# Optimization experiments

Measured on AMD Instinct MI355X. Metric: run time of the kernel, lower is better.

Reference implementation:

```python
import jax, jax.numpy as jnp
import numpy as np

B, T_FRAMES, N, D, H, HT = 2, 16, 256, 768, 12, 12
INNER = 2 * D  # ConditionedTransitionBlock expansion_factor=2

def _ln(x, eps=1e-5):
    m = jnp.mean(x, axis=-1, keepdims=True)
    v = jnp.var(x, axis=-1, keepdims=True)
    return (x - m) * jax.lax.rsqrt(v + eps)

def _adaln(a, s, snorm_w, scale_w, scale_b, shift_w):
    an = _ln(a)            # LayerNorm(dim), no affine
    sn = _ln(s) * snorm_w  # LayerNorm(dim_cond), weight only
    return jax.nn.sigmoid(sn @ scale_w + scale_b) * an + sn @ shift_w

def _forward(a, s, bias, timestamps,
             ada_snorm_w, ada_scale_w, ada_scale_b, ada_shift_w,
             pb_q_w, pb_q_b, pb_k_w, pb_v_w, pb_g_w, pb_o_w,
             op_w, op_b,
             tr_snorm_w, tr_scale_w, tr_scale_b, tr_shift_w,
             tr_gate_w, tr_ab_w, tr_ba_w, tr_out_w, tr_out_b,
             tmp_ln_w, tmp_ln_b, tmp_q_w, tmp_q_b, tmp_k_w, tmp_v_w,
             tmp_decay, tmp_o_w,
             mask, multiplicity, T):
    BT, Nn, Dd = a.shape
    Bb = BT // T
    dh = Dd // H
    # --- AdaLN ---
    b = _adaln(a, s, ada_snorm_w, ada_scale_w, ada_scale_b, ada_shift_w)
    # --- pair-bias spatial attention (compute_pair_bias=False: z already (B,N,N,H)) ---
    q = (b @ pb_q_w + pb_q_b).reshape(BT, Nn, H, dh)
    k = (b @ pb_k_w).reshape(BT, Nn, H, dh)
    v = (b @ pb_v_w).reshape(BT, Nn, H, dh)
    z = jnp.transpose(bias, (0, 3, 1, 2))     # (B, H, N, N)
    z = jnp.repeat(z, multiplicity, axis=0)   # expand over T -> (B*T, H, N, N)
    scores = jnp.einsum('bqhd,bkhd->bhqk', q, k) * (dh ** -0.5) + z
    scores = jnp.where(mask[:, None, None, :], scores, -1e6)
    attn = jax.nn.softmax(scores, axis=-1)
    o = jnp.einsum('bhqk,bkhd->bqhd', attn, v).reshape(BT, Nn, Dd)
    g = jax.nn.sigmoid(b @ pb_g_w)
    attn_out = (g * o) @ pb_o_w
    # gated output projection (sigmoid, weights init 0 / bias -2) multiplied into residual
    a = a + jax.nn.sigmoid(s @ op_w + op_b) * attn_out
    # --- temporal attention with decay over T frames ---
    x = a.reshape(Bb, T, Nn, Dd).transpose(0, 2, 1, 3)   # (B, N, T, D)
    h = _ln(x) * tmp_ln_w + tmp_ln_b
    dht = Dd // HT
    qt = (h @ tmp_q_w + tmp_q_b).reshape(Bb, Nn, T, HT, dht)
    kt = (h @ tmp_k_w).reshape(Bb, Nn, T, HT, dht)
    vt = (h @ tmp_v_w).reshape(Bb, Nn, T, HT, dht)
    dt = jnp.abs(timestamps[:, :, None] - timestamps[:, None, :])           # (B, T, T)
    tb = -jax.nn.softplus(tmp_decay)[None, :, None, None] * dt[:, None]     # (B, HT, T, T)
    sct = jnp.einsum('bnqhd,bnkhd->bnhqk', qt, kt) * (dht ** -0.5) + tb[:, None]
    att = jax.nn.softmax(sct, axis=-1)
    ot = jnp.einsum('bnhqk,bnkhd->bnqhd', att, vt).reshape(Bb, Nn, T, Dd) @ tmp_o_w
    x = x + ot  # residual inside temporal attention
    a = x.transpose(0, 2, 1, 3).reshape(BT, Nn, Dd)
    # --- conditioned transition (SwiGLU gated by sigmoid(Linear(s))) ---
    b2 = _adaln(a, s, tr_snorm_w, tr_scale_w, tr_scale_b, tr_shift_w)
    hid = jax.nn.silu(b2 @ tr_gate_w) * (b2 @ tr_ab_w)
    a = a + jax.nn.sigmoid(s @ tr_out_w + tr_out_b) * (hid @ tr_ba_w)
    return a  # post_layer_norm=False -> Identity

def setup_inputs():
    key = jax.random.key(0)
    ks = iter(jax.random.split(key, 48))
    f = lambda shape, sc=1.0: jax.random.normal(next(ks), shape, jnp.float32) * sc
    return {
        'a': f((B * T_FRAMES, N, D)),
        's': f((B * T_FRAMES, N, D)),
        'bias': f((B, N, N, H)),
        'mask': jnp.ones((B * T_FRAMES, N), dtype=bool),
        'timestamps': jnp.sort(jax.random.uniform(next(ks), (B, T_FRAMES)) * 10.0, axis=-1),
        'multiplicity': T_FRAMES,
        'T': T_FRAMES,
        'ada_snorm_w': jnp.ones((D,)), 'ada_scale_w': f((D, D), 0.02),
        'ada_scale_b': jnp.zeros((D,)), 'ada_shift_w': f((D, D), 0.02),
        'pb_q_w': f((D, D), 0.02), 'pb_q_b': jnp.zeros((D,)),
        'pb_k_w': f((D, D), 0.02), 'pb_v_w': f((D, D), 0.02),
        'pb_g_w': f((D, D), 0.02), 'pb_o_w': f((D, D), 0.02),
        'op_w': f((D, D), 0.02), 'op_b': jnp.full((D,), -2.0),
        'tr_snorm_w': jnp.ones((D,)), 'tr_scale_w': f((D, D), 0.02),
        'tr_scale_b': jnp.zeros((D,)), 'tr_shift_w': f((D, D), 0.02),
        'tr_gate_w': f((D, INNER), 0.02), 'tr_ab_w': f((D, INNER), 0.02),
        'tr_ba_w': f((INNER, D), 0.02),
        'tr_out_w': f((D, D), 0.02), 'tr_out_b': jnp.full((D,), -2.0),
        'tmp_ln_w': jnp.ones((D,)), 'tmp_ln_b': jnp.zeros((D,)),
        'tmp_q_w': f((D, D), 0.02), 'tmp_q_b': jnp.zeros((D,)),
        'tmp_k_w': f((D, D), 0.02), 'tmp_v_w': f((D, D), 0.02),
        'tmp_decay': jnp.full((HT,), 0.5), 'tmp_o_w': f((D, D), 0.02),
    }

def reference(a, s, bias, mask, timestamps, multiplicity, T,
              ada_snorm_w, ada_scale_w, ada_scale_b, ada_shift_w,
              pb_q_w, pb_q_b, pb_k_w, pb_v_w, pb_g_w, pb_o_w,
              op_w, op_b,
              tr_snorm_w, tr_scale_w, tr_scale_b, tr_shift_w,
              tr_gate_w, tr_ab_w, tr_ba_w, tr_out_w, tr_out_b,
              tmp_ln_w, tmp_ln_b, tmp_q_w, tmp_q_b, tmp_k_w, tmp_v_w,
              tmp_decay, tmp_o_w):
    return _forward(a, s, bias, timestamps,
                    ada_snorm_w, ada_scale_w, ada_scale_b, ada_shift_w,
                    pb_q_w, pb_q_b, pb_k_w, pb_v_w, pb_g_w, pb_o_w,
                    op_w, op_b,
                    tr_snorm_w, tr_scale_w, tr_scale_b, tr_shift_w,
                    tr_gate_w, tr_ab_w, tr_ba_w, tr_out_w, tr_out_b,
                    tmp_ln_w, tmp_ln_b, tmp_q_w, tmp_q_b, tmp_k_w, tmp_v_w,
                    tmp_decay, tmp_o_w,
                    mask, multiplicity, T)
```

## Files before the change

kernel.cpp:

```cpp
#include <hip/hip_runtime.h>

typedef short s16x8 __attribute__((ext_vector_type(8)));
typedef short s16x4 __attribute__((ext_vector_type(4)));
typedef float f32x4 __attribute__((ext_vector_type(4)));
typedef __bf16 bf16x8 __attribute__((ext_vector_type(8)));

__device__ __forceinline__ float bf2f(short u) {
  union { unsigned int i; float f; } c;
  c.i = ((unsigned int)(unsigned short)u) << 16;
  return c.f;
}
__device__ __forceinline__ short f2bf(float f) {
  union { float f; unsigned int i; } c; c.f = f;
  unsigned int r = c.i + 0x7FFFu + ((c.i >> 16) & 1u);
  return (short)(r >> 16);
}
__device__ __forceinline__ float sigmoidf_(float x) { return 1.f / (1.f + __expf(-x)); }

template <typename T>
__device__ __forceinline__ auto mfma_sel(T a, T b, f32x4 c, int)
    -> decltype(__builtin_amdgcn_mfma_f32_16x16x32_bf16(a, b, c, 0, 0, 0)) {
  return __builtin_amdgcn_mfma_f32_16x16x32_bf16(a, b, c, 0, 0, 0);
}
template <typename T>
__device__ __forceinline__ f32x4 mfma_sel(T a, T b, f32x4 c, long) {
  return __builtin_amdgcn_mfma_f32_16x16x32_bf16(
      __builtin_bit_cast(bf16x8, a), __builtin_bit_cast(bf16x8, b), c, 0, 0, 0);
}
__device__ __forceinline__ f32x4 MFMA16(s16x8 a, s16x8 b, f32x4 c) {
  return mfma_sel(a, b, c, 0);
}

__device__ __forceinline__ void gl2lds16(const void* g, void* l) {
  __builtin_amdgcn_global_load_lds(
      (const __attribute__((address_space(1))) unsigned int*)g,
      (__attribute__((address_space(3))) unsigned int*)l, 16, 0, 0);
}

#define OFF_WADA1    0u
#define OFF_WQKVG    2359296u
#define OFF_WO       7077888u
#define OFF_WGATES   8257536u
#define OFF_WTMPQKV  10616832u
#define OFF_WTMPO    14155776u
#define OFF_WADA2    15335424u
#define OFF_WTRANS   17694720u
#define OFF_WBA      22413312u
#define OFF_BIAS     24772608u
#define OFF_ZT       24812544u
#define OFF_AN1      31104000u
#define OFF_SN1      43686912u
#define OFF_SN2      56269824u
#define OFF_SBF      68852736u
#define OFF_CADA     81435648u
#define OFF_QKVG     106601472u
#define OFF_GATES    156933120u
#define OFF_OGO      182098944u
#define OFF_A1       194681856u

__global__ __launch_bounds__(256) void prep_all(
    const float* p0, const float* p1, const float* p2, const float* p3,
    const float* p4, const float* p5, const float* p6, const float* p7,
    const float* p8, const float* p9, const float* p10, const float* p11,
    const float* p12, const float* p13, const float* p14, const float* p15,
    const float* p16, const float* p17, short* wsb,
    const float* __restrict__ zsrc, const float* __restrict__ ada_scale_b,
    const float* __restrict__ pb_q_b, const float* __restrict__ op_b,
    const float* __restrict__ tr_out_b, const float* __restrict__ tmp_q_b,
    const float* __restrict__ tr_scale_b,
    float* __restrict__ biasbuf, short* __restrict__ zt,
    const float* __restrict__ a_in, const float* __restrict__ s_in,
    const float* __restrict__ lnw1, const float* __restrict__ lnw2,
    short* __restrict__ an1, short* __restrict__ sn1, short* __restrict__ sn2,
    short* __restrict__ sbf) {
  const int z = blockIdx.z;
  const int tid = threadIdx.y * 32 + threadIdx.x;
  if (z < 18) {
    struct E { int K, N, dst; };
    const E tab[18] = {
        {768, 768, 0},        {768, 768, 589824},
        {768, 768, 1179648},  {768, 768, 1769472},
        {768, 768, 2359296},  {768, 768, 2949120},
        {768, 768, 3538944},
        {768, 768, 4128768},  {768, 768, 4718592},
        {768, 768, 7667712},  {768, 768, 8257536},
        {768, 1536, 8847360}, {768, 1536, 10027008},
        {1536, 768, 11206656},
        {768, 768, 5308416},  {768, 768, 5898240}, {768, 768, 6488064},
        {768, 768, 7077888}};
    int K = tab[z].K, N = tab[z].N;
    int n0 = blockIdx.x << 5, k0 = blockIdx.y << 5;
    if (n0 >= N || k0 >= K) return;
    const float* src;
    switch (z) {
      case 0: src = p0; break;  case 1: src = p1; break;
      case 2: src = p2; break;  case 3: src = p3; break;
      case 4: src = p4; break;  case 5: src = p5; break;
      case 6: src = p6; break;  case 7: src = p7; break;
      case 8: src = p8; break;  case 9: src = p9; break;
      case 10: src = p10; break; case 11: src = p11; break;
      case 12: src = p12; break; case 13: src = p13; break;
      case 14: src = p14; break; case 15: src = p15; break;
      case 16: src = p16; break; default: src = p17; break;
    }
    short* dst = wsb + tab[z].dst;
    __shared__ float tile[32][33];
    int tx = threadIdx.x, ty = threadIdx.y;
#pragma unroll
    for (int j = 0; j < 4; j++)
      tile[ty + j * 8][tx] = src[(long)(k0 + ty + j * 8) * N + n0 + tx];
    __syncthreads();
#pragma unroll
    for (int j = 0; j < 4; j++)
      dst[(long)(n0 + ty + j * 8) * K + k0 + tx] = f2bf(tile[tx][ty + j * 8]);
  } else if (z == 18) {
    const int bid = blockIdx.y * 48 + blockIdx.x;
    if (bid < 512) {
      const int b = bid >> 8, qq = bid & 255;
      const float* src = zsrc + (long)bid * 3072 + tid * 12;
      f32x4 v0 = *(const f32x4*)(src);
      f32x4 v1 = *(const f32x4*)(src + 4);
      f32x4 v2 = *(const f32x4*)(src + 8);
      float vals[12] = {v0[0], v0[1], v0[2], v0[3], v1[0], v1[1],
                        v1[2], v1[3], v2[0], v2[1], v2[2], v2[3]};
#pragma unroll
      for (int h = 0; h < 12; h++)
        zt[(((long)(b * 12 + h) * 256 + qq) << 8) + tid] = f2bf(vals[h]);
    } else if (bid < 551) {
      int j = (bid - 512) * 256 + tid;
      if (j < 9984) {
        float v;
        if (j < 1536) v = (j < 768) ? ada_scale_b[j] : 0.f;
        else if (j < 4608) { int jj = j - 1536; v = (jj < 768) ? pb_q_b[jj] : 0.f; }
        else if (j < 6144) { int jj = j - 4608; v = (jj < 768) ? op_b[jj] : tr_out_b[jj - 768]; }
        else if (j < 8448) { int jj = j - 6144; v = (jj < 768) ? tmp_q_b[jj] : 0.f; }
        else { int jj = j - 8448; v = (jj < 768) ? tr_scale_b[jj] : 0.f; }
        biasbuf[j] = v;
      }
    }
  } else {
    const int bid = blockIdx.y * 48 + blockIdx.x;
    if (bid >= 2048) return;
    const int wave = tid >> 6, lane = tid & 63;
    const int row = (bid << 2) + wave;
    const float* ar = a_in + (long)row * 768;
    const float* sr = s_in + (long)row * 768;
    f32x4 av[3], sv[3];
    float s0 = 0, s1 = 0, s2 = 0, s3 = 0;
#pragma unroll
    for (int k = 0; k < 3; k++) {
      int col = (lane << 2) + (k << 8);
      av[k] = *(const f32x4*)(ar + col);
      sv[k] = *(const f32x4*)(sr + col);
#pragma unroll
      for (int e = 0; e < 4; e++) {
        s0 += av[k][e]; s1 += av[k][e] * av[k][e];
        s2 += sv[k][e]; s3 += sv[k][e] * sv[k][e];
      }
    }
#pragma unroll
    for (int o = 32; o; o >>= 1) {
      s0 += __shfl_xor(s0, o, 64); s1 += __shfl_xor(s1, o, 64);
      s2 += __shfl_xor(s2, o, 64); s3 += __shfl_xor(s3, o, 64);
    }
    const float inv768 = 1.f / 768.f;
    float ma = s0 * inv768, va = s1 * inv768 - ma * ma;
    float ia = rsqrtf(va + 1e-5f);
    float ms = s2 * inv768, vs = s3 * inv768 - ms * ms;
    float is_ = rsqrtf(vs + 1e-5f);
#pragma unroll
    for (int k = 0; k < 3; k++) {
      int col = (lane << 2) + (k << 8);
      long o = (long)row * 768 + col;
      s16x4 o1, o2, o3, o4;
#pragma unroll
      for (int e = 0; e < 4; e++) {
        o1[e] = f2bf((av[k][e] - ma) * ia);
        float sn = (sv[k][e] - ms) * is_;
        o2[e] = f2bf(sn * lnw1[col + e]);
        o3[e] = f2bf(sn * lnw2[col + e]);
        o4[e] = f2bf(sv[k][e]);
      }
      *(s16x4*)(an1 + o) = o1;
      *(s16x4*)(sn1 + o) = o2;
      *(s16x4*)(sn2 + o) = o3;
      *(s16x4*)(sbf + o) = o4;
    }
  }
}

__global__ __launch_bounds__(256) void ln_affine(
    const float* __restrict__ in, const float* __restrict__ w,
    const float* __restrict__ b, short* __restrict__ out) {
  const int wave = threadIdx.x >> 6, lane = threadIdx.x & 63;
  const int row = (blockIdx.x << 2) + wave;
  const float* xr = in + (long)row * 768;
  f32x4 xv[3];
  float s0 = 0, s1 = 0;
#pragma unroll
  for (int k = 0; k < 3; k++) {
    int col = (lane << 2) + (k << 8);
    xv[k] = *(const f32x4*)(xr + col);
#pragma unroll
    for (int e = 0; e < 4; e++) { s0 += xv[k][e]; s1 += xv[k][e] * xv[k][e]; }
  }
#pragma unroll
  for (int o = 32; o; o >>= 1) { s0 += __shfl_xor(s0, o, 64); s1 += __shfl_xor(s1, o, 64); }
  const float inv768 = 1.f / 768.f;
  float m = s0 * inv768, v = s1 * inv768 - m * m;
  float inv = rsqrtf(v + 1e-5f);
#pragma unroll
  for (int k = 0; k < 3; k++) {
    int col = (lane << 2) + (k << 8);
    s16x4 p;
#pragma unroll
    for (int e = 0; e < 4; e++) {
      float y = (xv[k][e] - m) * inv;
      if (w) y = y * w[col + e] + b[col + e];
      p[e] = f2bf(y);
    }
    *(s16x4*)(out + (long)row * 768 + col) = p;
  }
}

template <int EP>
__device__ __forceinline__ void dev_gemm_bt(
    short* lds,
    const short* __restrict__ A, const short* __restrict__ W,
    const float* __restrict__ bias, void* __restrict__ Cout,
    const float* __restrict__ res, const short* __restrict__ gate,
    int K, int ldA, int ldC, int gld) {
  short* sA = lds;
  short* sB = lds + 8192;
  const int tid = threadIdx.x;
  const int wave = tid >> 6, lane = tid & 63;
  const int m0 = blockIdx.y << 7;
  const int n0 = blockIdx.x << 7;
  const int wm = (wave & 1) << 6, wn = (wave >> 1) << 6;
  const int q = lane >> 4, r = lane & 15;
  f32x4 acc[4][4];
#pragma unroll
  for (int i = 0; i < 4; i++)
#pragma unroll
    for (int j = 0; j < 4; j++) acc[i][j] = (f32x4){0.f, 0.f, 0.f, 0.f};

  for (int kt = 0; kt < K; kt += 64) {
    __syncthreads();
#pragma unroll
    for (int t = 0; t < 4; t++) {
      int c = (t << 8) + tid;
      int m = c >> 3, kc = (c & 7) ^ (m & 7);
      gl2lds16(A + (long)(m0 + m) * ldA + kt + (kc << 3),
               sA + (((t << 8) + (wave << 6)) << 3));
      gl2lds16(W + (long)(n0 + m) * K + kt + (kc << 3),
               sB + (((t << 8) + (wave << 6)) << 3));
    }
    __syncthreads();
#pragma unroll
    for (int ks = 0; ks < 2; ks++) {
      s16x8 av[4], bv[4];
#pragma unroll
      for (int mt = 0; mt < 4; mt++) {
        int row = wm + (mt << 4) + r;
        int ch = ((ks << 2) + q) ^ (row & 7);
        av[mt] = *(const s16x8*)(sA + ((row << 3) + ch) * 8);
      }
#pragma unroll
      for (int nt = 0; nt < 4; nt++) {
        int row = wn + (nt << 4) + r;
        int ch = ((ks << 2) + q) ^ (row & 7);
        bv[nt] = *(const s16x8*)(sB + ((row << 3) + ch) * 8);
      }
#pragma unroll
      for (int mt = 0; mt < 4; mt++)
#pragma unroll
        for (int nt = 0; nt < 4; nt++)
          acc[mt][nt] = MFMA16(bv[nt], av[mt], acc[mt][nt]);
    }
  }
#pragma unroll
  for (int mt = 0; mt < 4; mt++) {
    const int gm = m0 + wm + (mt << 4) + r;
#pragma unroll
    for (int nt = 0; nt < 4; nt++) {
      const int gnb = n0 + wn + (nt << 4) + (q << 2);
      f32x4 v = acc[mt][nt];
      if (bias) {
        f32x4 b4 = *(const f32x4*)(bias + gnb);
        v += b4;
      }
      long o = (long)gm * ldC + gnb;
      if (EP == 0) {
        s16x4 p;
#pragma unroll
        for (int e = 0; e < 4; e++) p[e] = f2bf(v[e]);
        *(s16x4*)((short*)Cout + o) = p;
      } else if (EP == 1) {
        s16x4 p;
#pragma unroll
        for (int e = 0; e < 4; e++) p[e] = f2bf(sigmoidf_(v[e]));
        *(s16x4*)((short*)Cout + o) = p;
      } else if (EP == 2) {
        f32x4 r4 = *(const f32x4*)(res + o);
        *(f32x4*)((float*)Cout + o) = r4 + v;
      } else {
        f32x4 r4 = *(const f32x4*)(res + o);
        s16x4 g4 = *(const s16x4*)(gate + (long)gm * gld + gnb);
        f32x4 out;
#pragma unroll
        for (int e = 0; e < 4; e++) out[e] = r4[e] + bf2f(g4[e]) * v[e];
        *(f32x4*)((float*)Cout + o) = out;
      }
    }
  }
}

template <int MODE>
__device__ __forceinline__ void dev_gemm_dual(
    short* lds,
    const short* __restrict__ A, const short* __restrict__ W, int woff2,
    const float* __restrict__ bias, const short* __restrict__ an,
    short* __restrict__ out, int ldO) {
  short* sA = lds;
  short* sB1 = lds + 8192;
  short* sB2 = lds + 12288;
  const int tid = threadIdx.x;
  const int wave = tid >> 6, lane = tid & 63;
  const int m0 = blockIdx.y << 7;
  const int n0 = blockIdx.x << 6;
  const int wm = (wave & 1) << 6, wn = (wave >> 1) << 5;
  const int q = lane >> 4, r = lane & 15;
  f32x4 acc1[4][2], acc2[4][2];
#pragma unroll
  for (int i = 0; i < 4; i++)
#pragma unroll
    for (int j = 0; j < 2; j++) {
      acc1[i][j] = (f32x4){0.f, 0.f, 0.f, 0.f};
      acc2[i][j] = (f32x4){0.f, 0.f, 0.f, 0.f};
    }

  for (int kt = 0; kt < 768; kt += 64) {
    __syncthreads();
#pragma unroll
    for (int t = 0; t < 4; t++) {
      int c = (t << 8) + tid;
      int m = c >> 3, kc = (c & 7) ^ (m & 7);
      gl2lds16(A + (long)(m0 + m) * 768 + kt + (kc << 3),
               sA + (((t << 8) + (wave << 6)) << 3));
    }
#pragma unroll
    for (int t = 0; t < 2; t++) {
      int c = (t << 8) + tid;
      int rb = c >> 3, kc = (c & 7) ^ (rb & 7);
      gl2lds16(W + (long)(n0 + rb) * 768 + kt + (kc << 3),
               sB1 + (((t << 8) + (wave << 6)) << 3));
      gl2lds16(W + (long)(woff2 + n0 + rb) * 768 + kt + (kc << 3),
               sB2 + (((t << 8) + (wave << 6)) << 3));
    }
    __syncthreads();
#pragma unroll
    for (int ks = 0; ks < 2; ks++) {
      s16x8 av[4], b1[2], b2[2];
#pragma unroll
      for (int mt = 0; mt < 4; mt++) {
        int row = wm + (mt << 4) + r;
        int ch = ((ks << 2) + q) ^ (row & 7);
        av[mt] = *(const s16x8*)(sA + ((row << 3) + ch) * 8);
      }
#pragma unroll
      for (int nt = 0; nt < 2; nt++) {
        int row = wn + (nt << 4) + r;
        int ch = ((ks << 2) + q) ^ (row & 7);
        b1[nt] = *(const s16x8*)(sB1 + ((row << 3) + ch) * 8);
        b2[nt] = *(const s16x8*)(sB2 + ((row << 3) + ch) * 8);
      }
#pragma unroll
      for (int mt = 0; mt < 4; mt++)
#pragma unroll
        for (int nt = 0; nt < 2; nt++) {
          acc1[mt][nt] = MFMA16(b1[nt], av[mt], acc1[mt][nt]);
          acc2[mt][nt] = MFMA16(b2[nt], av[mt], acc2[mt][nt]);
        }
    }
  }
#pragma unroll
  for (int mt = 0; mt < 4; mt++) {
    const int gm = m0 + wm + (mt << 4) + r;
#pragma unroll
    for (int nt = 0; nt < 2; nt++) {
      const int gnb = n0 + wn + (nt << 4) + (q << 2);
      s16x4 p;
      if (MODE == 0) {
        f32x4 b4 = *(const f32x4*)(bias + gnb);
        s16x4 an4 = *(const s16x4*)(an + (long)gm * 768 + gnb);
#pragma unroll
        for (int e = 0; e < 4; e++)
          p[e] = f2bf(sigmoidf_(acc1[mt][nt][e] + b4[e]) * bf2f(an4[e]) +
                      acc2[mt][nt][e]);
      } else {
#pragma unroll
        for (int e = 0; e < 4; e++) {
          float x = acc1[mt][nt][e];
          p[e] = f2bf(x * sigmoidf_(x) * acc2[mt][nt][e]);
        }
      }
      *(s16x4*)(out + (long)gm * ldO + gnb) = p;
    }
  }
}

template <int EP>
__global__ __launch_bounds__(256) void gemm_bt(
    const short* __restrict__ A, const short* __restrict__ W,
    const float* __restrict__ bias, void* __restrict__ Cout,
    const float* __restrict__ res, const short* __restrict__ gate,
    int K, int ldA, int ldC, int gld) {
  __shared__ short lds[16384];
  dev_gemm_bt<EP>(lds, A, W, bias, Cout, res, gate, K, ldA, ldC, gld);
}

template <int MODE>
__global__ __launch_bounds__(256) void gemm_dual(
    const short* __restrict__ A, const short* __restrict__ W, int woff2,
    const float* __restrict__ bias, const short* __restrict__ an,
    short* __restrict__ out, int ldO) {
  __shared__ short lds[16384];
  dev_gemm_dual<MODE>(lds, A, W, woff2, bias, an, out, ldO);
}

__global__ __launch_bounds__(256) void gemm_pair(
    const short* __restrict__ sbf, const short* __restrict__ wgates,
    const float* __restrict__ bias_g, short* __restrict__ gates,
    const short* __restrict__ sn1, const short* __restrict__ wada1,
    const float* __restrict__ bias_a, const short* __restrict__ an1,
    short* __restrict__ outb) {
  __shared__ short lds[16384];
  if (blockIdx.z == 0)
    dev_gemm_bt<1>(lds, sbf, wgates, bias_g, (void*)gates, nullptr, nullptr,
                   768, 768, 1536, 0);
  else
    dev_gemm_dual<0>(lds, sn1, wada1, 768, bias_a, an1, outb, 768);
}

__global__ __launch_bounds__(256) void attn_spatial(
    const short* __restrict__ qkvg, const short* __restrict__ zt, short* __restrict__ ogo) {
  __shared__ short sKP[256 * 64];
  __shared__ short sVt[64 * 256];
  const int tid = threadIdx.x;
  const int wave = tid >> 6, lane = tid & 63;
  const int qt = blockIdx.x, h = blockIdx.y, bt = blockIdx.z;
  const int b = bt >> 4;
  const int q0 = qt << 6;
  const long rowbase = (long)bt << 8;
  const int hoff = h << 6;

#pragma unroll
  for (int t = 0; t < 8; t++) {
    int c = (t << 8) + tid;
    int tok = c >> 3, kc = (c & 7) ^ (tok & 7);
    *(s16x8*)(sKP + (c << 3)) =
        *(const s16x8*)(qkvg + (rowbase + tok) * 3072 + 768 + hoff + (kc << 3));
  }
#pragma unroll
  for (int t = 0; t < 8; t++) {
    int u = (t << 8) + tid;
    int tok = u >> 3, dc = u & 7;
    s16x8 v8 = *(const s16x8*)(qkvg + (rowbase + tok) * 3072 + 1536 + hoff + (dc << 3));
#pragma unroll
    for (int e = 0; e < 8; e++) {
      int d = (dc << 3) + e;
      int ch = (tok >> 3) ^ (d & 7);
      sVt[((d << 5) + ch) * 8 + (tok & 7)] = v8[e];
    }
  }
  __syncthreads();

  const int q = lane >> 4, cc = lane & 15;
  f32x4 acc[16];
#pragma unroll
  for (int i = 0; i < 16; i++) acc[i] = (f32x4){0.f, 0.f, 0.f, 0.f};
  {
    const int arow = (wave << 4) + cc;
    const short* qrow = qkvg + (rowbase + q0 + arow) * 3072 + hoff;
#pragma unroll
    for (int ks = 0; ks < 2; ks++) {
      s16x8 av = *(const s16x8*)(qrow + (ks << 5) + (q << 3));
#pragma unroll
      for (int nt = 0; nt < 16; nt++) {
        int tok = (nt << 4) + cc;
        int chb = ((ks << 2) + q) ^ (tok & 7);
        s16x8 bv = *(const s16x8*)(sKP + ((tok << 3) + chb) * 8);
        acc[nt] = MFMA16(av, bv, acc[nt]);
      }
    }
  }
  const short* ztb = zt + (((long)(b * 12 + h) * 256 + q0 + (wave << 4)) << 8);
#pragma unroll
  for (int reg = 0; reg < 4; reg++) {
    int lr = (q << 2) + reg;
    float mx = -3.0e38f;
#pragma unroll
    for (int nt = 0; nt < 16; nt++) {
      float v = acc[nt][reg] * 0.125f + bf2f(ztb[lr * 256 + (nt << 4) + cc]);
      acc[nt][reg] = v;
      mx = fmaxf(mx, v);
    }
    mx = fmaxf(mx, __shfl_xor(mx, 1, 16));
    mx = fmaxf(mx, __shfl_xor(mx, 2, 16));
    mx = fmaxf(mx, __shfl_xor(mx, 4, 16));
    mx = fmaxf(mx, __shfl_xor(mx, 8, 16));
    float sum = 0.f;
#pragma unroll
    for (int nt = 0; nt < 16; nt++) {
      float e = __expf(acc[nt][reg] - mx);
      acc[nt][reg] = e; sum += e;
    }
    sum += __shfl_xor(sum, 1, 16);
    sum += __shfl_xor(sum, 2, 16);
    sum += __shfl_xor(sum, 4, 16);
    sum += __shfl_xor(sum, 8, 16);
    float inv = 1.f / sum;
#pragma unroll
    for (int nt = 0; nt < 16; nt++) acc[nt][reg] *= inv;
  }
  __syncthreads();
#pragma unroll
  for (int nt = 0; nt < 16; nt++) {
#pragma unroll
    for (int reg = 0; reg < 4; reg++) {
      int rP = (wave << 4) + (q << 2) + reg;
      int col = (nt << 4) + cc;
      int ch = (col >> 3) ^ (rP & 7);
      sKP[((rP << 5) + ch) * 8 + (col & 7)] = f2bf(acc[nt][reg]);
    }
  }
  __syncthreads();
  f32x4 oacc[4];
#pragma unroll
  for (int i = 0; i < 4; i++) oacc[i] = (f32x4){0.f, 0.f, 0.f, 0.f};
  const int prow = (wave << 4) + cc;
#pragma unroll
  for (int ksi = 0; ksi < 8; ksi++) {
    int cha = ((ksi << 2) + q) ^ (prow & 7);
    s16x8 pa = *(const s16x8*)(sKP + ((prow << 5) + cha) * 8);
#pragma unroll
    for (int dt = 0; dt < 4; dt++) {
      int d = (dt << 4) + cc;
      int chv = ((ksi << 2) + q) ^ (d & 7);
      s16x8 bv = *(const s16x8*)(sVt + ((d << 5) + chv) * 8);
      oacc[dt] = MFMA16(pa, bv, oacc[dt]);
    }
  }
#pragma unroll
  for (int dt = 0; dt < 4; dt++) {
#pragma unroll
    for (int reg = 0; reg < 4; reg++) {
      int rowt = q0 + (wave << 4) + (q << 2) + reg;
      int dcol = (dt << 4) + cc;
      long grow = rowbase + rowt;
      float gl = bf2f(qkvg[grow * 3072 + 2304 + hoff + dcol]);
      ogo[grow * 768 + hoff + dcol] = f2bf(oacc[dt][reg] * sigmoidf_(gl));
    }
  }
}

__global__ __launch_bounds__(256) void attn_temporal(
    const short* __restrict__ qkvt, const float* __restrict__ ts,
    const float* __restrict__ decay_raw, short* __restrict__ out) {
  __shared__ short sKV[16 * 1544];
  const int bn = blockIdx.x;
  const int b = bn >> 8, n = bn & 255;
  const int tid = threadIdx.x;
#pragma unroll
  for (int t = 0; t < 12; t++) {
    int u = t * 256 + tid;
    int row = u / 192, cc = u % 192;
    *(s16x8*)(sKV + row * 1544 + cc * 8) =
        *(const s16x8*)(qkvt + ((long)(b * 16 + row) * 256 + n) * 2304 + 768 + cc * 8);
  }
  __syncthreads();
  const int h = tid >> 4, tq = tid & 15;
  if (h < 12) {
    const int hoff = h << 6;
    float dec = log1pf(__expf(decay_raw[h]));
    float tsq = ts[b * 16 + tq];
    s16x8 qv[8];
    const short* qrow = qkvt + ((long)(b * 16 + tq) * 256 + n) * 2304 + hoff;
#pragma unroll
    for (int dc = 0; dc < 8; dc++) qv[dc] = *(const s16x8*)(qrow + dc * 8);
    float sc[16];
#pragma unroll
    for (int tk = 0; tk < 16; tk++) {
      float dot = 0.f;
#pragma unroll
      for (int dc = 0; dc < 8; dc++) {
        s16x8 kv = *(const s16x8*)(sKV + tk * 1544 + hoff + dc * 8);
#pragma unroll
        for (int e = 0; e < 8; e++) dot += bf2f(qv[dc][e]) * bf2f(kv[e]);
      }
      sc[tk] = dot * 0.125f - dec * fabsf(tsq - ts[b * 16 + tk]);
    }
    float mx = sc[0];
#pragma unroll
    for (int tk = 1; tk < 16; tk++) mx = fmaxf(mx, sc[tk]);
    float sum = 0.f;
#pragma unroll
    for (int tk = 0; tk < 16; tk++) { sc[tk] = __expf(sc[tk] - mx); sum += sc[tk]; }
    float inv = 1.f / sum;
    float oa[64];
#pragma unroll
    for (int d = 0; d < 64; d++) oa[d] = 0.f;
#pragma unroll
    for (int tk = 0; tk < 16; tk++) {
      float wgt = sc[tk] * inv;
#pragma unroll
      for (int dc = 0; dc < 8; dc++) {
        s16x8 vv = *(const s16x8*)(sKV + tk * 1544 + 768 + hoff + dc * 8);
#pragma unroll
        for (int e = 0; e < 8; e++) oa[dc * 8 + e] += wgt * bf2f(vv[e]);
      }
    }
    long orow = (long)(b * 16 + tq) * 256 + n;
#pragma unroll
    for (int dc = 0; dc < 8; dc++) {
      s16x8 o8;
#pragma unroll
      for (int e = 0; e < 8; e++) o8[e] = f2bf(oa[dc * 8 + e]);
      *(s16x8*)(out + orow * 768 + hoff + dc * 8) = o8;
    }
  }
}

extern "C" void kernel_launch(void* const* d_in, const int* in_sizes, int n_in,
                              void* d_out, int out_size, void* d_ws, size_t ws_size,
                              hipStream_t stream) {
  (void)in_sizes; (void)n_in; (void)out_size; (void)ws_size;
  const float* a_in      = (const float*)d_in[0];
  const float* s_in      = (const float*)d_in[1];
  const float* bias_in   = (const float*)d_in[2];
  const float* ts        = (const float*)d_in[4];
  const float* ada_snorm = (const float*)d_in[7];
  const float* ada_scale_w = (const float*)d_in[8];
  const float* ada_scale_b = (const float*)d_in[9];
  const float* ada_shift_w = (const float*)d_in[10];
  const float* pb_q_w = (const float*)d_in[11];
  const float* pb_q_b = (const float*)d_in[12];
  const float* pb_k_w = (const float*)d_in[13];
  const float* pb_v_w = (const float*)d_in[14];
  const float* pb_g_w = (const float*)d_in[15];
  const float* pb_o_w = (const float*)d_in[16];
  const float* op_w = (const float*)d_in[17];
  const float* op_b = (const float*)d_in[18];
  const float* tr_snorm = (const float*)d_in[19];
  const float* tr_scale_w = (const float*)d_in[20];
  const float* tr_scale_b = (const float*)d_in[21];
  const float* tr_shift_w = (const float*)d_in[22];
  const float* tr_gate_w = (const float*)d_in[23];
  const float* tr_ab_w = (const float*)d_in[24];
  const float* tr_ba_w = (const float*)d_in[25];
  const float* tr_out_w = (const float*)d_in[26];
  const float* tr_out_b = (const float*)d_in[27];
  const float* tmp_ln_w = (const float*)d_in[28];
  const float* tmp_ln_b = (const float*)d_in[29];
  const float* tmp_q_w = (const float*)d_in[30];
  const float* tmp_q_b = (const float*)d_in[31];
  const float* tmp_k_w = (const float*)d_in[32];
  const float* tmp_v_w = (const float*)d_in[33];
  const float* tmp_decay = (const float*)d_in[34];
  const float* tmp_o_w = (const float*)d_in[35];

  char* ws = (char*)d_ws;
  short* W16 = (short*)ws;
  short* WADA1 = (short*)(ws + OFF_WADA1);
  short* WQKVG = (short*)(ws + OFF_WQKVG);
  short* WO = (short*)(ws + OFF_WO);
  short* WGATES = (short*)(ws + OFF_WGATES);
  short* WTMPQKV = (short*)(ws + OFF_WTMPQKV);
  short* WTMPO = (short*)(ws + OFF_WTMPO);
  short* WADA2 = (short*)(ws + OFF_WADA2);
  short* WTRANS = (short*)(ws + OFF_WTRANS);
  short* WBA = (short*)(ws + OFF_WBA);
  float* BIASB = (float*)(ws + OFF_BIAS);
  short* ZT = (short*)(ws + OFF_ZT);
  short* AN1 = (short*)(ws + OFF_AN1);
  short* SN1 = (short*)(ws + OFF_SN1);
  short* SN2 = (short*)(ws + OFF_SN2);
  short* SBF = (short*)(ws + OFF_SBF);
  short* CADA = (short*)(ws + OFF_CADA);
  short* QKVG = (short*)(ws + OFF_QKVG);
  short* GATES = (short*)(ws + OFF_GATES);
  short* OGO = (short*)(ws + OFF_OGO);
  float* A1F = (float*)(ws + OFF_A1);
  float* OUTF = (float*)d_out;

  prep_all<<<dim3(48, 48, 20), dim3(32, 8, 1), 0, stream>>>(
      ada_scale_w, ada_shift_w, pb_q_w, pb_k_w, pb_v_w, pb_g_w, pb_o_w,
      op_w, tr_out_w, tr_scale_w, tr_shift_w, tr_gate_w, tr_ab_w, tr_ba_w,
      tmp_q_w, tmp_k_w, tmp_v_w, tmp_o_w, W16,
      bias_in, ada_scale_b, pb_q_b, op_b, tr_out_b, tmp_q_b, tr_scale_b,
      BIASB, ZT,
      a_in, s_in, ada_snorm, tr_snorm, AN1, SN1, SN2, SBF);
  gemm_pair<<<dim3(12, 64, 2), 256, 0, stream>>>(
      SBF, WGATES, BIASB + 4608, GATES, SN1, WADA1, BIASB + 0, AN1, SBF);
  gemm_bt<0><<<dim3(24, 64), 256, 0, stream>>>(SBF, WQKVG, BIASB + 1536, QKVG,
                                               nullptr, nullptr, 768, 768, 3072, 0);
  attn_spatial<<<dim3(4, 12, 32), 256, 0, stream>>>(QKVG, ZT, OGO);
  gemm_bt<3><<<dim3(6, 64), 256, 0, stream>>>(OGO, WO, nullptr, A1F, a_in, GATES,
                                              768, 768, 768, 1536);
  ln_affine<<<2048, 256, 0, stream>>>(A1F, tmp_ln_w, tmp_ln_b, AN1);
  gemm_bt<0><<<dim3(18, 64), 256, 0, stream>>>(AN1, WTMPQKV, BIASB + 6144, QKVG,
                                               nullptr, nullptr, 768, 768, 2304, 0);
  attn_temporal<<<512, 256, 0, stream>>>(QKVG, ts, tmp_decay, OGO);
  gemm_bt<2><<<dim3(6, 64), 256, 0, stream>>>(OGO, WTMPO, nullptr, A1F, A1F, nullptr,
                                              768, 768, 768, 0);
  ln_affine<<<2048, 256, 0, stream>>>(A1F, nullptr, nullptr, SN1);
  gemm_dual<0><<<dim3(12, 64), 256, 0, stream>>>(SN2, WADA2, 768, BIASB + 8448, SN1,
                                                 SBF, 768);
  gemm_dual<1><<<dim3(24, 64), 256, 0, stream>>>(SBF, WTRANS, 1536, nullptr, nullptr,
                                                 CADA, 1536);
  gemm_bt<3><<<dim3(6, 64), 256, 0, stream>>>(CADA, WBA, nullptr, OUTF, A1F,
                                              GATES + 768, 1536, 1536, 768, 1536);
}
```

Measured before the change: 680.3 us.

## Store GEMM operands in MFMA-fragment packed layout and drop LDS staging

Activation and weight matrices are written by the producers in a packed 16-row x 8-column tile layout that matches the MFMA fragment order. The GEMM kernels then load each fragment straight from global memory with one 16-byte vector load per lane, with no LDS staging and no __syncthreads. This removes the LDS round trip and the barriers. In exchange, the A and B tiles are no longer shared through LDS, so every wave fetches its own fragments from global/L2 with no software prefetch, which may raise global traffic and expose load latency.

```diff
diff --git a/kernel.cpp b/kernel.cpp
--- a/kernel.cpp
+++ b/kernel.cpp
@@ -31,10 +31,8 @@
   return mfma_sel(a, b, c, 0);
 }
 
-__device__ __forceinline__ void gl2lds16(const void* g, void* l) {
-  __builtin_amdgcn_global_load_lds(
-      (const __attribute__((address_space(1))) unsigned int*)g,
-      (__attribute__((address_space(3))) unsigned int*)l, 16, 0, 0);
+__device__ __forceinline__ long upk(int m, int c, int nu) {
+  return ((long)(m >> 4) * nu + (c >> 3)) * 128 + ((m & 15) << 3) + (c & 7);
 }
 
 #define OFF_WADA1    0u
@@ -104,6 +102,7 @@
       case 16: src = p16; break; default: src = p17; break;
     }
     short* dst = wsb + tab[z].dst;
+    const int ku = K >> 3;
     __shared__ float tile[32][33];
     int tx = threadIdx.x, ty = threadIdx.y;
 #pragma unroll
@@ -111,8 +110,10 @@
       tile[ty + j * 8][tx] = src[(long)(k0 + ty + j * 8) * N + n0 + tx];
     __syncthreads();
 #pragma unroll
-    for (int j = 0; j < 4; j++)
-      dst[(long)(n0 + ty + j * 8) * K + k0 + tx] = f2bf(tile[tx][ty + j * 8]);
+    for (int j = 0; j < 4; j++) {
+      int n = n0 + ty + j * 8, k = k0 + tx;
+      dst[upk(n, k, ku)] = f2bf(tile[tx][ty + j * 8]);
+    }
   } else if (z == 18) {
     const int bid = blockIdx.y * 48 + blockIdx.x;
     if (bid < 512) {
@@ -171,7 +172,7 @@
 #pragma unroll
     for (int k = 0; k < 3; k++) {
       int col = (lane << 2) + (k << 8);
-      long o = (long)row * 768 + col;
+      long o = upk(row, col, 96);
       s16x4 o1, o2, o3, o4;
 #pragma unroll
       for (int e = 0; e < 4; e++) {
@@ -219,25 +220,30 @@
       if (w) y = y * w[col + e] + b[col + e];
       p[e] = f2bf(y);
     }
-    *(s16x4*)(out + (long)row * 768 + col) = p;
+    *(s16x4*)(out + upk(row, col, 96)) = p;
   }
 }
 
 template <int EP>
-__device__ __forceinline__ void dev_gemm_bt(
-    short* lds,
+__device__ __forceinline__ void dev_gemm_pk(
     const short* __restrict__ A, const short* __restrict__ W,
     const float* __restrict__ bias, void* __restrict__ Cout,
     const float* __restrict__ res, const short* __restrict__ gate,
-    int K, int ldA, int ldC, int gld) {
-  short* sA = lds;
-  short* sB = lds + 8192;
+    int K, int ldC, int gld) {
   const int tid = threadIdx.x;
   const int wave = tid >> 6, lane = tid & 63;
-  const int m0 = blockIdx.y << 7;
-  const int n0 = blockIdx.x << 7;
+  const int m0 = blockIdx.y << 7, n0 = blockIdx.x << 7;
   const int wm = (wave & 1) << 6, wn = (wave >> 1) << 6;
   const int q = lane >> 4, r = lane & 15;
+  const int ku = K >> 3;
+  const short* ap[4];
+  const short* bp[4];
+#pragma unroll
+  for (int mt = 0; mt < 4; mt++)
+    ap[mt] = A + (long)(((m0 + wm) >> 4) + mt) * ku * 128 + (lane << 3);
+#pragma unroll
+  for (int nt = 0; nt < 4; nt++)
+    bp[nt] = W + (long)(((n0 + wn) >> 4) + nt) * ku * 128 + (lane << 3);
   f32x4 acc[4][4];
 #pragma unroll
   for (int i = 0; i < 4; i++)
@@ -245,38 +251,25 @@
     for (int j = 0; j < 4; j++) acc[i][j] = (f32x4){0.f, 0.f, 0.f, 0.f};
 
   for (int kt = 0; kt < K; kt += 64) {
-    __syncthreads();
-#pragma unroll
-    for (int t = 0; t < 4; t++) {
-      int c = (t << 8) + tid;
-      int m = c >> 3, kc = (c & 7) ^ (m & 7);
-      gl2lds16(A + (long)(m0 + m) * ldA + kt + (kc << 3),
-               sA + (((t << 8) + (wave << 6)) << 3));
-      gl2lds16(W + (long)(n0 + m) * K + kt + (kc << 3),
-               sB + (((t << 8) + (wave << 6)) << 3));
-    }
-    __syncthreads();
 #pragma unroll
     for (int ks = 0; ks < 2; ks++) {
       s16x8 av[4], bv[4];
 #pragma unroll
-      for (int mt = 0; mt < 4; mt++) {
-        int row = wm + (mt << 4) + r;
-        int ch = ((ks << 2) + q) ^ (row & 7);
-        av[mt] = *(const s16x8*)(sA + ((row << 3) + ch) * 8);
-      }
-#pragma unroll
-      for (int nt = 0; nt < 4; nt++) {
-        int row = wn + (nt << 4) + r;
-        int ch = ((ks << 2) + q) ^ (row & 7);
-        bv[nt] = *(const s16x8*)(sB + ((row << 3) + ch) * 8);
-      }
+      for (int mt = 0; mt < 4; mt++)
+        av[mt] = *(const s16x8*)(ap[mt] + (ks << 9));
+#pragma unroll
+      for (int nt = 0; nt < 4; nt++)
+        bv[nt] = *(const s16x8*)(bp[nt] + (ks << 9));
 #pragma unroll
       for (int mt = 0; mt < 4; mt++)
 #pragma unroll
         for (int nt = 0; nt < 4; nt++)
           acc[mt][nt] = MFMA16(bv[nt], av[mt], acc[mt][nt]);
     }
+#pragma unroll
+    for (int mt = 0; mt < 4; mt++) ap[mt] += 1024;
+#pragma unroll
+    for (int nt = 0; nt < 4; nt++) bp[nt] += 1024;
   }
 #pragma unroll
   for (int mt = 0; mt < 4; mt++) {
@@ -316,20 +309,27 @@
 }
 
 template <int MODE>
-__device__ __forceinline__ void dev_gemm_dual(
-    short* lds,
-    const short* __restrict__ A, const short* __restrict__ W, int woff2,
-    const float* __restrict__ bias, const short* __restrict__ an,
-    short* __restrict__ out, int ldO) {
-  short* sA = lds;
-  short* sB1 = lds + 8192;
-  short* sB2 = lds + 12288;
+__device__ __forceinline__ void dev_gemm_dual_pk(
+    const short* __restrict__ A, const short* __restrict__ W1,
+    const short* __restrict__ W2, const float* __restrict__ bias,
+    const short* __restrict__ an, short* __restrict__ out, int nuO) {
   const int tid = threadIdx.x;
   const int wave = tid >> 6, lane = tid & 63;
-  const int m0 = blockIdx.y << 7;
-  const int n0 = blockIdx.x << 6;
+  const int m0 = blockIdx.y << 7, n0 = blockIdx.x << 6;
   const int wm = (wave & 1) << 6, wn = (wave >> 1) << 5;
   const int q = lane >> 4, r = lane & 15;
+  const short* ap[4];
+  const short* b1p[2];
+  const short* b2p[2];
+#pragma unroll
+  for (int mt = 0; mt < 4; mt++)
+    ap[mt] = A + (long)(((m0 + wm) >> 4) + mt) * 96 * 128 + (lane << 3);
+#pragma unroll
+  for (int nt = 0; nt < 2; nt++) {
+    long nb = (long)(((n0 + wn) >> 4) + nt) * 96 * 128 + (lane << 3);
+    b1p[nt] = W1 + nb;
+    b2p[nt] = W2 + nb;
+  }
   f32x4 acc1[4][2], acc2[4][2];
 #pragma unroll
   for (int i = 0; i < 4; i++)
@@ -338,41 +338,17 @@
       acc1[i][j] = (f32x4){0.f, 0.f, 0.f, 0.f};
       acc2[i][j] = (f32x4){0.f, 0.f, 0.f, 0.f};
     }
-
   for (int kt = 0; kt < 768; kt += 64) {
-    __syncthreads();
-#pragma unroll
-    for (int t = 0; t < 4; t++) {
-      int c = (t << 8) + tid;
-      int m = c >> 3, kc = (c & 7) ^ (m & 7);
-      gl2lds16(A + (long)(m0 + m) * 768 + kt + (kc << 3),
-               sA + (((t << 8) + (wave << 6)) << 3));
-    }
-#pragma unroll
-    for (int t = 0; t < 2; t++) {
-      int c = (t << 8) + tid;
-      int rb = c >> 3, kc = (c & 7) ^ (rb & 7);
-      gl2lds16(W + (long)(n0 + rb) * 768 + kt + (kc << 3),
-               sB1 + (((t << 8) + (wave << 6)) << 3));
-      gl2lds16(W + (long)(woff2 + n0 + rb) * 768 + kt + (kc << 3),
-               sB2 + (((t << 8) + (wave << 6)) << 3));
-    }
-    __syncthreads();
 #pragma unroll
     for (int ks = 0; ks < 2; ks++) {
       s16x8 av[4], b1[2], b2[2];
 #pragma unroll
-      for (int mt = 0; mt < 4; mt++) {
-        int row = wm + (mt << 4) + r;
-        int ch = ((ks << 2) + q) ^ (row & 7);
-        av[mt] = *(const s16x8*)(sA + ((row << 3) + ch) * 8);
-      }
+      for (int mt = 0; mt < 4; mt++)
+        av[mt] = *(const s16x8*)(ap[mt] + (ks << 9));
 #pragma unroll
       for (int nt = 0; nt < 2; nt++) {
-        int row = wn + (nt << 4) + r;
-        int ch = ((ks << 2) + q) ^ (row & 7);
-        b1[nt] = *(const s16x8*)(sB1 + ((row << 3) + ch) * 8);
-        b2[nt] = *(const s16x8*)(sB2 + ((row << 3) + ch) * 8);
+        b1[nt] = *(const s16x8*)(b1p[nt] + (ks << 9));
+        b2[nt] = *(const s16x8*)(b2p[nt] + (ks << 9));
       }
 #pragma unroll
       for (int mt = 0; mt < 4; mt++)
@@ -382,6 +358,10 @@
           acc2[mt][nt] = MFMA16(b2[nt], av[mt], acc2[mt][nt]);
         }
     }
+#pragma unroll
+    for (int mt = 0; mt < 4; mt++) ap[mt] += 1024;
+#pragma unroll
+    for (int nt = 0; nt < 2; nt++) { b1p[nt] += 1024; b2p[nt] += 1024; }
   }
 #pragma unroll
   for (int mt = 0; mt < 4; mt++) {
@@ -392,7 +372,7 @@
       s16x4 p;
       if (MODE == 0) {
         f32x4 b4 = *(const f32x4*)(bias + gnb);
-        s16x4 an4 = *(const s16x4*)(an + (long)gm * 768 + gnb);
+        s16x4 an4 = *(const s16x4*)(an + upk(gm, gnb, 96));
 #pragma unroll
         for (int e = 0; e < 4; e++)
           p[e] = f2bf(sigmoidf_(acc1[mt][nt][e] + b4[e]) * bf2f(an4[e]) +
@@ -404,28 +384,26 @@
           p[e] = f2bf(x * sigmoidf_(x) * acc2[mt][nt][e]);
         }
       }
-      *(s16x4*)(out + (long)gm * ldO + gnb) = p;
+      *(s16x4*)(out + upk(gm, gnb, nuO)) = p;
     }
   }
 }
 
 template <int EP>
-__global__ __launch_bounds__(256) void gemm_bt(
+__global__ __launch_bounds__(256) void gemm_pk(
     const short* __restrict__ A, const short* __restrict__ W,
     const float* __restrict__ bias, void* __restrict__ Cout,
     const float* __restrict__ res, const short* __restrict__ gate,
-    int K, int ldA, int ldC, int gld) {
-  __shared__ short lds[16384];
-  dev_gemm_bt<EP>(lds, A, W, bias, Cout, res, gate, K, ldA, ldC, gld);
+    int K, int ldC, int gld) {
+  dev_gemm_pk<EP>(A, W, bias, Cout, res, gate, K, ldC, gld);
 }
 
 template <int MODE>
-__global__ __launch_bounds__(256) void gemm_dual(
-    const short* __restrict__ A, const short* __restrict__ W, int woff2,
-    const float* __restrict__ bias, const short* __restrict__ an,
-    short* __restrict__ out, int ldO) {
-  __shared__ short lds[16384];
-  dev_gemm_dual<MODE>(lds, A, W, woff2, bias, an, out, ldO);
+__global__ __launch_bounds__(256) void gemm_dual_pk(
+    const short* __restrict__ A, const short* __restrict__ W1,
+    const short* __restrict__ W2, const float* __restrict__ bias,
+    const short* __restrict__ an, short* __restrict__ out, int nuO) {
+  dev_gemm_dual_pk<MODE>(A, W1, W2, bias, an, out, nuO);
 }
 
 __global__ __launch_bounds__(256) void gemm_pair(
@@ -434,12 +412,12 @@
     const short* __restrict__ sn1, const short* __restrict__ wada1,
     const float* __restrict__ bias_a, const short* __restrict__ an1,
     short* __restrict__ outb) {
-  __shared__ short lds[16384];
   if (blockIdx.z == 0)
-    dev_gemm_bt<1>(lds, sbf, wgates, bias_g, (void*)gates, nullptr, nullptr,
-                   768, 768, 1536, 0);
+    dev_gemm_pk<1>(sbf, wgates, bias_g, (void*)gates, nullptr, nullptr,
+                   768, 1536, 0);
   else
-    dev_gemm_dual<0>(lds, sn1, wada1, 768, bias_a, an1, outb, 768);
+    dev_gemm_dual_pk<0>(sn1, wada1, wada1 + (long)768 * 768, bias_a, an1,
+                        outb, 96);
 }
 
 __global__ __launch_bounds__(256) void attn_spatial(
@@ -559,7 +537,7 @@
       int dcol = (dt << 4) + cc;
       long grow = rowbase + rowt;
       float gl = bf2f(qkvg[grow * 3072 + 2304 + hoff + dcol]);
-      ogo[grow * 768 + hoff + dcol] = f2bf(oacc[dt][reg] * sigmoidf_(gl));
+      ogo[upk((int)grow, hoff + dcol, 96)] = f2bf(oacc[dt][reg] * sigmoidf_(gl));
     }
   }
 }
@@ -620,13 +598,13 @@
         for (int e = 0; e < 8; e++) oa[dc * 8 + e] += wgt * bf2f(vv[e]);
       }
     }
-    long orow = (long)(b * 16 + tq) * 256 + n;
+    int orow = (b * 16 + tq) * 256 + n;
 #pragma unroll
     for (int dc = 0; dc < 8; dc++) {
       s16x8 o8;
 #pragma unroll
       for (int e = 0; e < 8; e++) o8[e] = f2bf(oa[dc * 8 + e]);
-      *(s16x8*)(out + orow * 768 + hoff + dc * 8) = o8;
+      *(s16x8*)(out + upk(orow, hoff + (dc << 3), 96)) = o8;
     }
   }
 }
@@ -702,22 +680,22 @@
       a_in, s_in, ada_snorm, tr_snorm, AN1, SN1, SN2, SBF);
   gemm_pair<<<dim3(12, 64, 2), 256, 0, stream>>>(
       SBF, WGATES, BIASB + 4608, GATES, SN1, WADA1, BIASB + 0, AN1, SBF);
-  gemm_bt<0><<<dim3(24, 64), 256, 0, stream>>>(SBF, WQKVG, BIASB + 1536, QKVG,
-                                               nullptr, nullptr, 768, 768, 3072, 0);
+  gemm_pk<0><<<dim3(24, 64), 256, 0, stream>>>(SBF, WQKVG, BIASB + 1536, QKVG,
+                                               nullptr, nullptr, 768, 3072, 0);
   attn_spatial<<<dim3(4, 12, 32), 256, 0, stream>>>(QKVG, ZT, OGO);
-  gemm_bt<3><<<dim3(6, 64), 256, 0, stream>>>(OGO, WO, nullptr, A1F, a_in, GATES,
-                                              768, 768, 768, 1536);
+  gemm_pk<3><<<dim3(6, 64), 256, 0, stream>>>(OGO, WO, nullptr, A1F, a_in, GATES,
+                                              768, 768, 1536);
   ln_affine<<<2048, 256, 0, stream>>>(A1F, tmp_ln_w, tmp_ln_b, AN1);
-  gemm_bt<0><<<dim3(18, 64), 256, 0, stream>>>(AN1, WTMPQKV, BIASB + 6144, QKVG,
-                                               nullptr, nullptr, 768, 768, 2304, 0);
+  gemm_pk<0><<<dim3(18, 64), 256, 0, stream>>>(AN1, WTMPQKV, BIASB + 6144, QKVG,
+                                               nullptr, nullptr, 768, 2304, 0);
   attn_temporal<<<512, 256, 0, stream>>>(QKVG, ts, tmp_decay, OGO);
-  gemm_bt<2><<<dim3(6, 64), 256, 0, stream>>>(OGO, WTMPO, nullptr, A1F, A1F, nullptr,
-                                              768, 768, 768, 0);
+  gemm_pk<2><<<dim3(6, 64), 256, 0, stream>>>(OGO, WTMPO, nullptr, A1F, A1F,
+                                              nullptr, 768, 768, 0);
   ln_affine<<<2048, 256, 0, stream>>>(A1F, nullptr, nullptr, SN1);
-  gemm_dual<0><<<dim3(12, 64), 256, 0, stream>>>(SN2, WADA2, 768, BIASB + 8448, SN1,
-                                                 SBF, 768);
-  gemm_dual<1><<<dim3(24, 64), 256, 0, stream>>>(SBF, WTRANS, 1536, nullptr, nullptr,
-                                                 CADA, 1536);
-  gemm_bt<3><<<dim3(6, 64), 256, 0, stream>>>(CADA, WBA, nullptr, OUTF, A1F,
-                                              GATES + 768, 1536, 1536, 768, 1536);
-}
+  gemm_dual_pk<0><<<dim3(12, 64), 256, 0, stream>>>(
+      SN2, WADA2, WADA2 + (long)768 * 768, BIASB + 8448, SN1, SBF, 96);
+  gemm_dual_pk<1><<<dim3(24, 64), 256, 0, stream>>>(
+      SBF, WTRANS, WTRANS + (long)1536 * 768, nullptr, nullptr, CADA, 192);
+  gemm_pk<3><<<dim3(6, 64), 256, 0, stream>>>(CADA, WBA, nullptr, OUTF, A1F,
+                                              GATES + 768, 1536, 768, 1536);
+}
```

Result: slower. 697.7 us (+2.6%).
